# Kernel optimization log

Measured on AMD Instinct MI355X. Metric: run time of the kernel, lower is better.

The kernel has to match this reference:

```python
import jax, jax.numpy as jnp
import numpy as np

N_NODES = 100000
N_EDGES = 800000
N_IN = 256
N_H = 128


def setup_inputs() -> dict:
    key = jax.random.key(0)
    ks = jax.random.split(key, 8)
    x_1 = jax.random.normal(ks[0], (1, N_NODES, N_IN), dtype=jnp.float32)
    x_2 = jax.random.normal(ks[1], (1, N_NODES, N_IN), dtype=jnp.float32)
    edge_index = jax.random.randint(ks[2], (2, N_EDGES), 0, N_NODES, dtype=jnp.int32)
    edge_weight = jax.random.uniform(ks[3], (N_EDGES,), dtype=jnp.float32)
    # xavier-uniform-ish init for fc weight (stored as [in, out])
    lim = float(np.sqrt(6.0 / (N_IN + N_H)))
    W_gcn = jax.random.uniform(ks[4], (N_IN, N_H), minval=-lim, maxval=lim, dtype=jnp.float32)
    gcn_bias = jnp.zeros((N_H,), dtype=jnp.float32)
    prelu_a = jnp.full((1,), 0.25, dtype=jnp.float32)  # PReLU default slope
    lim2 = float(np.sqrt(1.0 / N_H))
    lin_W = jax.random.uniform(ks[5], (N_H, N_H), minval=-lim2, maxval=lim2, dtype=jnp.float32)
    lin_b = jax.random.uniform(ks[6], (N_H,), minval=-lim2, maxval=lim2, dtype=jnp.float32)
    return {
        "x_1": x_1, "x_2": x_2, "edge_index": edge_index, "edge_weight": edge_weight,
        "W_gcn": W_gcn, "gcn_bias": gcn_bias, "prelu_a": prelu_a,
        "lin_W": lin_W, "lin_b": lin_b,
    }


def _prelu(x, a):
    return jnp.where(x >= 0, x, a * x)


def _gcn(feat, edge_index, edge_weight, W, b, a, n_nodes):
    # feat: [1, N, n_in] -> h: [N, n_h]
    h = jnp.squeeze(feat, 0) @ W
    row, col = edge_index[0], edge_index[1]
    # spmm: out[i] = sum_{e: row_e = i} w_e * h[col_e]
    msg = edge_weight[:, None] * h[col]            # [E, n_h]
    agg = jax.ops.segment_sum(msg, row, num_segments=n_nodes)  # [N, n_h]
    return _prelu(agg + b, a)                      # [N, n_h]


def reference(x_1, x_2, edge_index, edge_weight, W_gcn, gcn_bias, prelu_a, lin_W, lin_b):
    n = x_1.shape[1]
    h_1 = _gcn(x_1, edge_index, edge_weight, W_gcn, gcn_bias, prelu_a, n)
    h_2 = _gcn(x_2, edge_index, edge_weight, W_gcn, gcn_bias, prelu_a, n)
    z_1 = (h_1 @ lin_W + lin_b).sum(1)   # [N]
    z_2 = (h_2 @ lin_W + lin_b).sum(1)   # [N]
    return jnp.concatenate((z_1, z_2), 0)  # [2N]
```

## Files before the change

### kernel.cpp

```cpp
#include <hip/hip_runtime.h>

#define N_NODES 100000
#define N_EDGES 800000
#define N_IN    256
#define N_H     128
#define M_TOT   (2 * N_NODES)

typedef __bf16 bfx8 __attribute__((ext_vector_type(8)));
typedef unsigned short u16x8 __attribute__((ext_vector_type(8)));
typedef float fx4 __attribute__((ext_vector_type(4)));

__device__ inline unsigned short f2bf(float f) {
    union { float f; unsigned u; } v; v.f = f;
    return (unsigned short)((v.u + 0x7FFF + ((v.u >> 16) & 1)) >> 16);
}
__device__ inline float bf2f(unsigned short s) {
    union { unsigned u; float f; } v; v.u = ((unsigned)s) << 16;
    return v.f;
}

#define WT_S 264
#define NGB  1563
#define NSB  1563

__global__ __launch_bounds__(512, 2) void gemm_scatter_kernel(
        const float* __restrict__ x1, const float* __restrict__ x2,
        const unsigned short* __restrict__ wT,
        unsigned short* __restrict__ hb,
        const int* __restrict__ ei, const float* __restrict__ ew,
        int* __restrict__ cursor, int2* __restrict__ edata) {
    const int t = threadIdx.x;
    if (blockIdx.x >= NGB) {
        int e = (blockIdx.x - NGB) * 512 + t;
        if (e < N_EDGES) {
            int row = ei[e];
            int pos = atomicAdd(cursor + row, 1);
            edata[pos] = make_int2(ei[N_EDGES + e] * N_H, __float_as_int(ew[e]));
        }
        return;
    }
    __shared__ unsigned short wl[N_H * WT_S];
#pragma unroll
    for (int i = 0; i < 8; ++i) {
        int f  = t + i * 512;
        int n  = f >> 5;
        int kp = (f & 31) * 8;
        *(u16x8*)(wl + n * WT_S + kp) = *(const u16x8*)(wT + n * N_IN + kp);
    }
    __syncthreads();

    const int wave = t >> 6, lane = t & 63;
    const int quad = lane >> 4, l16 = lane & 15;
    const int mw = blockIdx.x * 128 + wave * 16;
    if (mw >= M_TOT) return;
    const float* x = (mw < N_NODES) ? x1 : x2;
    const int mrow = (mw < N_NODES) ? mw : mw - N_NODES;

    fx4 acc[8];
#pragma unroll
    for (int c = 0; c < 8; ++c) acc[c] = (fx4){0.f, 0.f, 0.f, 0.f};

    const float* xrow = x + (size_t)(mrow + l16) * N_IN;
#pragma unroll
    for (int kk = 0; kk < N_IN; kk += 32) {
        float4 a0 = *(const float4*)(xrow + kk + quad * 8);
        float4 a1 = *(const float4*)(xrow + kk + quad * 8 + 4);
        u16x8 au;
        au[0] = f2bf(a0.x); au[1] = f2bf(a0.y); au[2] = f2bf(a0.z); au[3] = f2bf(a0.w);
        au[4] = f2bf(a1.x); au[5] = f2bf(a1.y); au[6] = f2bf(a1.z); au[7] = f2bf(a1.w);
        bfx8 af = __builtin_bit_cast(bfx8, au);
#pragma unroll
        for (int c = 0; c < 8; ++c) {
            bfx8 bf = *(const bfx8*)(wl + (size_t)(c * 16 + l16) * WT_S + kk + quad * 8);
            acc[c] = __builtin_amdgcn_mfma_f32_16x16x32_bf16(af, bf, acc[c], 0, 0, 0);
        }
    }
#pragma unroll
    for (int c = 0; c < 8; ++c)
#pragma unroll
        for (int r = 0; r < 4; ++r)
            hb[(size_t)(mw + quad * 4 + r) * N_H + c * 16 + l16] = f2bf(acc[c][r]);
}

#define HIST_BLKS 3125
__global__ __launch_bounds__(256) void prep_kernel(const int* __restrict__ ei,
                                                   int* __restrict__ deg,
                                                   const float* __restrict__ W,
                                                   unsigned short* __restrict__ wT,
                                                   const float* __restrict__ linW,
                                                   const float* __restrict__ linb,
                                                   float* __restrict__ wsum) {
    const int t = threadIdx.x;
    if (blockIdx.x < HIST_BLKS) {
        int e = blockIdx.x * 256 + t;
        if (e < N_EDGES) atomicAdd(deg + ei[e], 1);
    } else if (blockIdx.x < HIST_BLKS + 32) {
        int kb = (blockIdx.x - HIST_BLKS) * 8;
#pragma unroll
        for (int p = 0; p < 4; ++p) {
            int idx = p * 256 + t;
            int k = kb + (idx >> 7), n = idx & 127;
            wT[(size_t)n * N_IN + k] = f2bf(W[(size_t)k * N_H + n]);
        }
    } else {
        int j = t;
        if (j < N_H) {
            float s = 0.f;
            for (int o = 0; o < N_H; ++o) s += linW[j * N_H + o];
            wsum[j] = s;
        }
        if (j == N_H) {
            float s = 0.f;
            for (int o = 0; o < N_H; ++o) s += linb[o];
            wsum[N_H] = s;
        }
    }
}

__global__ __launch_bounds__(256) void scan1_kernel(const int* __restrict__ deg,
                                                    int* __restrict__ part,
                                                    int* __restrict__ bsum) {
    __shared__ int s[256];
    int g = blockIdx.x * 256 + threadIdx.x;
    int v = (g < N_NODES) ? deg[g] : 0;
    s[threadIdx.x] = v;
    __syncthreads();
#pragma unroll
    for (int off = 1; off < 256; off <<= 1) {
        int t = (threadIdx.x >= off) ? s[threadIdx.x - off] : 0;
        __syncthreads();
        s[threadIdx.x] += t;
        __syncthreads();
    }
    if (g < N_NODES) part[g] = s[threadIdx.x] - v;
    if (threadIdx.x == 255) bsum[blockIdx.x] = s[255];
}

#define NBLK_SCAN 391
__global__ void scan2_kernel(int* __restrict__ bsum) {
    __shared__ int s[512];
    int v = (threadIdx.x < NBLK_SCAN) ? bsum[threadIdx.x] : 0;
    s[threadIdx.x] = v;
    __syncthreads();
#pragma unroll
    for (int off = 1; off < 512; off <<= 1) {
        int t = (threadIdx.x >= off) ? s[threadIdx.x - off] : 0;
        __syncthreads();
        s[threadIdx.x] += t;
        __syncthreads();
    }
    if (threadIdx.x < NBLK_SCAN) bsum[threadIdx.x] = s[threadIdx.x] - v;
}

__global__ __launch_bounds__(256) void scan3_kernel(const int* __restrict__ part,
                                                    const int* __restrict__ bsum,
                                                    int* __restrict__ off,
                                                    int* __restrict__ cursor) {
    int g = blockIdx.x * 256 + threadIdx.x;
    if (g < N_NODES) {
        int o = part[g] + bsum[blockIdx.x];
        off[g] = o;
        cursor[g] = o;
    }
    if (g == 0) off[N_NODES] = N_EDGES;
}

__global__ __launch_bounds__(256) void gcn_seg_kernel(const int* __restrict__ off,
                                                      const int2* __restrict__ edata,
                                                      const unsigned short* __restrict__ hb,
                                                      const float* __restrict__ gcn_bias,
                                                      const float* __restrict__ prelu_a,
                                                      const float* __restrict__ wsum,
                                                      float* __restrict__ zout) {
    const int wave = threadIdx.x >> 6, lane = threadIdx.x & 63;
    const int node = blockIdx.x * 4 + wave;
    const unsigned short* h1 = hb;
    const unsigned short* h2 = hb + (size_t)N_NODES * N_H;
    const int s = __builtin_amdgcn_readfirstlane(off[node]);
    const int e = __builtin_amdgcn_readfirstlane(off[node + 1]);
    const int l2 = lane * 2;
    float a0 = 0.f, a1 = 0.f;
    float b0 = 0.f, b1 = 0.f;
    int i = s;
    for (; i + 1 < e; i += 2) {
        int2 E0 = edata[i], E1 = edata[i + 1];
        float w0 = __int_as_float(E0.y), w1 = __int_as_float(E1.y);
        ushort2 p10 = *(const ushort2*)(h1 + E0.x + l2);
        ushort2 p20 = *(const ushort2*)(h2 + E0.x + l2);
        ushort2 p11 = *(const ushort2*)(h1 + E1.x + l2);
        ushort2 p21 = *(const ushort2*)(h2 + E1.x + l2);
        a0 += w0 * bf2f(p10.x) + w1 * bf2f(p11.x);
        a1 += w0 * bf2f(p10.y) + w1 * bf2f(p11.y);
        b0 += w0 * bf2f(p20.x) + w1 * bf2f(p21.x);
        b1 += w0 * bf2f(p20.y) + w1 * bf2f(p21.y);
    }
    if (i < e) {
        int2 E0 = edata[i];
        float w0 = __int_as_float(E0.y);
        ushort2 p10 = *(const ushort2*)(h1 + E0.x + l2);
        ushort2 p20 = *(const ushort2*)(h2 + E0.x + l2);
        a0 += w0 * bf2f(p10.x);
        a1 += w0 * bf2f(p10.y);
        b0 += w0 * bf2f(p20.x);
        b1 += w0 * bf2f(p20.y);
    }
    const float alpha = prelu_a[0];
    const float g0 = gcn_bias[l2], g1 = gcn_bias[l2 + 1];
    const float q0 = wsum[l2],     q1 = wsum[l2 + 1];
    float v0 = a0 + g0, v1 = a1 + g1;
    float u0 = b0 + g0, u1 = b1 + g1;
    v0 = (v0 >= 0.f) ? v0 : alpha * v0;
    v1 = (v1 >= 0.f) ? v1 : alpha * v1;
    u0 = (u0 >= 0.f) ? u0 : alpha * u0;
    u1 = (u1 >= 0.f) ? u1 : alpha * u1;
    float s1 = v0 * q0 + v1 * q1;
    float s2 = u0 * q0 + u1 * q1;
#pragma unroll
    for (int o = 32; o; o >>= 1) {
        s1 += __shfl_down(s1, o, 64);
        s2 += __shfl_down(s2, o, 64);
    }
    if (lane == 0) {
        zout[node]           = s1 + wsum[128];
        zout[node + N_NODES] = s2 + wsum[128];
    }
}

extern "C" void kernel_launch(void* const* d_in, const int* in_sizes, int n_in,
                              void* d_out, int out_size, void* d_ws, size_t ws_size,
                              hipStream_t stream) {
    const float* x1 = (const float*)d_in[0];
    const float* x2 = (const float*)d_in[1];
    const int*   ei = (const int*)d_in[2];
    const float* ew = (const float*)d_in[3];
    const float* Wg = (const float*)d_in[4];
    const float* gb = (const float*)d_in[5];
    const float* pa = (const float*)d_in[6];
    const float* lW = (const float*)d_in[7];
    const float* lb = (const float*)d_in[8];
    float* zout = (float*)d_out;

    unsigned short* hb   = (unsigned short*)d_ws;
    int2*  edata  = (int2*)(hb + (size_t)M_TOT * N_H);
    unsigned short* wT   = (unsigned short*)(edata + N_EDGES);
    int*   deg    = (int*)(wT + N_IN * N_H);
    int*   part   = deg + 100096;
    int*   off    = part + 100096;
    int*   cursor = off + 100096;
    int*   bsum   = cursor + 100096;
    float* wsum   = (float*)(bsum + 512);

    hipMemsetAsync(deg, 0, (size_t)N_NODES * sizeof(int), stream);
    prep_kernel<<<HIST_BLKS + 33, 256, 0, stream>>>(ei, deg, Wg, wT, lW, lb, wsum);
    scan1_kernel<<<NBLK_SCAN, 256, 0, stream>>>(deg, part, bsum);
    scan2_kernel<<<1, 512, 0, stream>>>(bsum);
    scan3_kernel<<<NBLK_SCAN, 256, 0, stream>>>(part, bsum, off, cursor);
    gemm_scatter_kernel<<<NGB + NSB, 512, 0, stream>>>(x1, x2, wT, hb,
                                                       ei, ew, cursor, edata);
    gcn_seg_kernel<<<N_NODES / 4, 256, 0, stream>>>(off, edata, hb, gb, pa, wsum, zout);
}
```

Baseline: 392.3 us.

## Interleave h1/h2 rows, split scatter from GEMM, fold scan2 into scan3

Stores the two branch projections interleaved per node (256-wide rows), so each gathered neighbour gives one contiguous 512-byte read covering both graphs. Each half-wave handles one branch with ushort4 loads and a 4-edge unrolled loop using two accumulator sets. The edge scatter moves out of the fused GEMM kernel into its own launch. scan2 is removed by having each scan3 block sum the preceding block totals itself, which makes later blocks do redundant reduction work. The GEMM launch bound rises to 4 blocks per CU.

```diff
diff --git a/kernel.cpp b/kernel.cpp
--- a/kernel.cpp
+++ b/kernel.cpp
@@ -5,6 +5,7 @@
 #define N_IN    256
 #define N_H     128
 #define M_TOT   (2 * N_NODES)
+#define HB_ROW  256
 
 typedef __bf16 bfx8 __attribute__((ext_vector_type(8)));
 typedef unsigned short u16x8 __attribute__((ext_vector_type(8)));
@@ -21,25 +22,13 @@
 
 #define WT_S 264
 #define NGB  1563
-#define NSB  1563
-
-__global__ __launch_bounds__(512, 2) void gemm_scatter_kernel(
+
+__global__ __launch_bounds__(512, 4) void gemm_kernel(
         const float* __restrict__ x1, const float* __restrict__ x2,
         const unsigned short* __restrict__ wT,
-        unsigned short* __restrict__ hb,
-        const int* __restrict__ ei, const float* __restrict__ ew,
-        int* __restrict__ cursor, int2* __restrict__ edata) {
+        unsigned short* __restrict__ hb) {
+    __shared__ unsigned short wl[N_H * WT_S];
     const int t = threadIdx.x;
-    if (blockIdx.x >= NGB) {
-        int e = (blockIdx.x - NGB) * 512 + t;
-        if (e < N_EDGES) {
-            int row = ei[e];
-            int pos = atomicAdd(cursor + row, 1);
-            edata[pos] = make_int2(ei[N_EDGES + e] * N_H, __float_as_int(ew[e]));
-        }
-        return;
-    }
-    __shared__ unsigned short wl[N_H * WT_S];
 #pragma unroll
     for (int i = 0; i < 8; ++i) {
         int f  = t + i * 512;
@@ -53,8 +42,9 @@
     const int quad = lane >> 4, l16 = lane & 15;
     const int mw = blockIdx.x * 128 + wave * 16;
     if (mw >= M_TOT) return;
-    const float* x = (mw < N_NODES) ? x1 : x2;
-    const int mrow = (mw < N_NODES) ? mw : mw - N_NODES;
+    const int half = (mw < N_NODES) ? 0 : 1;
+    const float* x = half ? x2 : x1;
+    const int mrow = half ? mw - N_NODES : mw;
 
     fx4 acc[8];
 #pragma unroll
@@ -79,7 +69,8 @@
     for (int c = 0; c < 8; ++c)
 #pragma unroll
         for (int r = 0; r < 4; ++r)
-            hb[(size_t)(mw + quad * 4 + r) * N_H + c * 16 + l16] = f2bf(acc[c][r]);
+            hb[(size_t)(mrow + quad * 4 + r) * HB_ROW + half * N_H + c * 16 + l16] =
+                f2bf(acc[c][r]);
 }
 
 #define HIST_BLKS 3125
@@ -137,32 +128,40 @@
 }
 
 #define NBLK_SCAN 391
-__global__ void scan2_kernel(int* __restrict__ bsum) {
-    __shared__ int s[512];
-    int v = (threadIdx.x < NBLK_SCAN) ? bsum[threadIdx.x] : 0;
-    s[threadIdx.x] = v;
-    __syncthreads();
-#pragma unroll
-    for (int off = 1; off < 512; off <<= 1) {
-        int t = (threadIdx.x >= off) ? s[threadIdx.x - off] : 0;
-        __syncthreads();
-        s[threadIdx.x] += t;
-        __syncthreads();
-    }
-    if (threadIdx.x < NBLK_SCAN) bsum[threadIdx.x] = s[threadIdx.x] - v;
-}
-
 __global__ __launch_bounds__(256) void scan3_kernel(const int* __restrict__ part,
                                                     const int* __restrict__ bsum,
                                                     int* __restrict__ off,
                                                     int* __restrict__ cursor) {
-    int g = blockIdx.x * 256 + threadIdx.x;
+    __shared__ int red[256];
+    const int t = threadIdx.x;
+    int acc = 0;
+    for (int j = t; j < (int)blockIdx.x; j += 256) acc += bsum[j];
+    red[t] = acc;
+    __syncthreads();
+#pragma unroll
+    for (int o = 128; o; o >>= 1) {
+        if (t < o) red[t] += red[t + o];
+        __syncthreads();
+    }
+    const int prefix = red[0];
+    int g = blockIdx.x * 256 + t;
     if (g < N_NODES) {
-        int o = part[g] + bsum[blockIdx.x];
+        int o = part[g] + prefix;
         off[g] = o;
         cursor[g] = o;
     }
     if (g == 0) off[N_NODES] = N_EDGES;
+}
+
+__global__ __launch_bounds__(256) void scatter_kernel(const int* __restrict__ ei,
+                                                      const float* __restrict__ ew,
+                                                      int* __restrict__ cursor,
+                                                      int2* __restrict__ edata) {
+    int e = blockIdx.x * 256 + threadIdx.x;
+    if (e >= N_EDGES) return;
+    int row = ei[e];
+    int pos = atomicAdd(cursor + row, 1);
+    edata[pos] = make_int2(ei[N_EDGES + e] * HB_ROW, __float_as_int(ew[e]));
 }
 
 __global__ __launch_bounds__(256) void gcn_seg_kernel(const int* __restrict__ off,
@@ -174,56 +173,55 @@
                                                       float* __restrict__ zout) {
     const int wave = threadIdx.x >> 6, lane = threadIdx.x & 63;
     const int node = blockIdx.x * 4 + wave;
-    const unsigned short* h1 = hb;
-    const unsigned short* h2 = hb + (size_t)N_NODES * N_H;
+    const int half = lane >> 5;
+    const int fl   = (lane & 31) * 4;
+    const int o8   = half * N_H + fl;
     const int s = __builtin_amdgcn_readfirstlane(off[node]);
     const int e = __builtin_amdgcn_readfirstlane(off[node + 1]);
-    const int l2 = lane * 2;
-    float a0 = 0.f, a1 = 0.f;
-    float b0 = 0.f, b1 = 0.f;
+    float p0 = 0.f, p1 = 0.f, p2 = 0.f, p3 = 0.f;
+    float q0 = 0.f, q1 = 0.f, q2 = 0.f, q3 = 0.f;
     int i = s;
-    for (; i + 1 < e; i += 2) {
-        int2 E0 = edata[i], E1 = edata[i + 1];
+    for (; i + 4 <= e; i += 4) {
+        int2 E0 = edata[i], E1 = edata[i + 1], E2 = edata[i + 2], E3 = edata[i + 3];
+        ushort4 h0 = *(const ushort4*)(hb + E0.x + o8);
+        ushort4 h1 = *(const ushort4*)(hb + E1.x + o8);
+        ushort4 h2 = *(const ushort4*)(hb + E2.x + o8);
+        ushort4 h3 = *(const ushort4*)(hb + E3.x + o8);
         float w0 = __int_as_float(E0.y), w1 = __int_as_float(E1.y);
-        ushort2 p10 = *(const ushort2*)(h1 + E0.x + l2);
-        ushort2 p20 = *(const ushort2*)(h2 + E0.x + l2);
-        ushort2 p11 = *(const ushort2*)(h1 + E1.x + l2);
-        ushort2 p21 = *(const ushort2*)(h2 + E1.x + l2);
-        a0 += w0 * bf2f(p10.x) + w1 * bf2f(p11.x);
-        a1 += w0 * bf2f(p10.y) + w1 * bf2f(p11.y);
-        b0 += w0 * bf2f(p20.x) + w1 * bf2f(p21.x);
-        b1 += w0 * bf2f(p20.y) + w1 * bf2f(p21.y);
-    }
-    if (i < e) {
+        float w2 = __int_as_float(E2.y), w3 = __int_as_float(E3.y);
+        p0 += w0 * bf2f(h0.x) + w1 * bf2f(h1.x);
+        p1 += w0 * bf2f(h0.y) + w1 * bf2f(h1.y);
+        p2 += w0 * bf2f(h0.z) + w1 * bf2f(h1.z);
+        p3 += w0 * bf2f(h0.w) + w1 * bf2f(h1.w);
+        q0 += w2 * bf2f(h2.x) + w3 * bf2f(h3.x);
+        q1 += w2 * bf2f(h2.y) + w3 * bf2f(h3.y);
+        q2 += w2 * bf2f(h2.z) + w3 * bf2f(h3.z);
+        q3 += w2 * bf2f(h2.w) + w3 * bf2f(h3.w);
+    }
+    for (; i < e; ++i) {
         int2 E0 = edata[i];
         float w0 = __int_as_float(E0.y);
-        ushort2 p10 = *(const ushort2*)(h1 + E0.x + l2);
-        ushort2 p20 = *(const ushort2*)(h2 + E0.x + l2);
-        a0 += w0 * bf2f(p10.x);
-        a1 += w0 * bf2f(p10.y);
-        b0 += w0 * bf2f(p20.x);
-        b1 += w0 * bf2f(p20.y);
-    }
+        ushort4 h0 = *(const ushort4*)(hb + E0.x + o8);
+        p0 += w0 * bf2f(h0.x);
+        p1 += w0 * bf2f(h0.y);
+        p2 += w0 * bf2f(h0.z);
+        p3 += w0 * bf2f(h0.w);
+    }
+    p0 += q0; p1 += q1; p2 += q2; p3 += q3;
+
     const float alpha = prelu_a[0];
-    const float g0 = gcn_bias[l2], g1 = gcn_bias[l2 + 1];
-    const float q0 = wsum[l2],     q1 = wsum[l2 + 1];
-    float v0 = a0 + g0, v1 = a1 + g1;
-    float u0 = b0 + g0, u1 = b1 + g1;
+    float4 gb4 = *(const float4*)(gcn_bias + fl);
+    float4 ws4 = *(const float4*)(wsum + fl);
+    float v0 = p0 + gb4.x, v1 = p1 + gb4.y, v2 = p2 + gb4.z, v3 = p3 + gb4.w;
     v0 = (v0 >= 0.f) ? v0 : alpha * v0;
     v1 = (v1 >= 0.f) ? v1 : alpha * v1;
-    u0 = (u0 >= 0.f) ? u0 : alpha * u0;
-    u1 = (u1 >= 0.f) ? u1 : alpha * u1;
-    float s1 = v0 * q0 + v1 * q1;
-    float s2 = u0 * q0 + u1 * q1;
-#pragma unroll
-    for (int o = 32; o; o >>= 1) {
-        s1 += __shfl_down(s1, o, 64);
-        s2 += __shfl_down(s2, o, 64);
-    }
-    if (lane == 0) {
-        zout[node]           = s1 + wsum[128];
-        zout[node + N_NODES] = s2 + wsum[128];
-    }
+    v2 = (v2 >= 0.f) ? v2 : alpha * v2;
+    v3 = (v3 >= 0.f) ? v3 : alpha * v3;
+    float sres = v0 * ws4.x + v1 * ws4.y + v2 * ws4.z + v3 * ws4.w;
+#pragma unroll
+    for (int o = 16; o; o >>= 1) sres += __shfl_down(sres, o, 32);
+    if ((lane & 31) == 0)
+        zout[node + half * N_NODES] = sres + wsum[128];
 }
 
 extern "C" void kernel_launch(void* const* d_in, const int* in_sizes, int n_in,
@@ -241,7 +239,7 @@
     float* zout = (float*)d_out;
 
     unsigned short* hb   = (unsigned short*)d_ws;
-    int2*  edata  = (int2*)(hb + (size_t)M_TOT * N_H);
+    int2*  edata  = (int2*)(hb + (size_t)N_NODES * HB_ROW);
     unsigned short* wT   = (unsigned short*)(edata + N_EDGES);
     int*   deg    = (int*)(wT + N_IN * N_H);
     int*   part   = deg + 100096;
@@ -253,9 +251,8 @@
     hipMemsetAsync(deg, 0, (size_t)N_NODES * sizeof(int), stream);
     prep_kernel<<<HIST_BLKS + 33, 256, 0, stream>>>(ei, deg, Wg, wT, lW, lb, wsum);
     scan1_kernel<<<NBLK_SCAN, 256, 0, stream>>>(deg, part, bsum);
-    scan2_kernel<<<1, 512, 0, stream>>>(bsum);
     scan3_kernel<<<NBLK_SCAN, 256, 0, stream>>>(part, bsum, off, cursor);
-    gemm_scatter_kernel<<<NGB + NSB, 512, 0, stream>>>(x1, x2, wT, hb,
-                                                       ei, ew, cursor, edata);
+    scatter_kernel<<<(N_EDGES + 255) / 256, 256, 0, stream>>>(ei, ew, cursor, edata);
+    gemm_kernel<<<NGB, 512, 0, stream>>>(x1, x2, wT, hb);
     gcn_seg_kernel<<<N_NODES / 4, 256, 0, stream>>>(off, edata, hb, gb, pa, wsum, zout);
 }
```

After: 399.6 us. No clear change (+1.8%).
